# Performance work log

Hardware: AMD Instinct MI355X
Metric: run time of the kernel (lower is better)

The kernel has to match this reference:

```python
import jax, jax.numpy as jnp
import numpy as np
from jax import lax

IMAGE_SIZE = 1280
STRIDE = 32
FMP = IMAGE_SIZE // STRIDE          # 40
BPC = 5                             # boxes per cell (5 anchors)
NUM_CLASSES = 80
NMS_THRESH = 0.5
CONF_THRESH = 0.3
N_BOX = FMP * FMP * BPC             # 8000 candidates
ANCHOR_SIZE = np.array([[17, 25], [55, 75], [92, 206], [202, 21], [289, 311]], dtype=np.float32)


def _make_anchors():
    # generate_anchors: per-cell (x,y) grid repeated for each of BPC anchors, tiled anchor wh
    ys, xs = jnp.meshgrid(jnp.arange(FMP, dtype=jnp.float32), jnp.arange(FMP, dtype=jnp.float32), indexing='ij')
    xy = jnp.stack([xs, ys], axis=-1).reshape(-1, 1, 2)                       # [HW,1,2]
    anchor_xy = jnp.broadcast_to(xy, (FMP * FMP, BPC, 2)).reshape(-1, 2)      # [N,2]
    anchor_wh = jnp.broadcast_to(jnp.asarray(ANCHOR_SIZE)[None], (FMP * FMP, BPC, 2)).reshape(-1, 2)
    return jnp.concatenate([anchor_xy, anchor_wh], axis=-1)                   # [N,4]


def setup_inputs() -> dict:
    key = jax.random.key(0)
    k = jax.random.split(key, 5)
    return {
        'cls_feat': jax.random.normal(k[0], (1, 512, FMP, FMP), jnp.float32),
        'reg_feat': jax.random.normal(k[1], (1, 512, FMP, FMP), jnp.float32),
        'w_obj': jax.random.normal(k[2], (BPC, 512), jnp.float32) * 0.02,
        'b_obj': jnp.zeros((BPC,), jnp.float32),
        'w_cls': jax.random.normal(k[3], (NUM_CLASSES * BPC, 512), jnp.float32) * 0.02,
        'b_cls': jnp.zeros((NUM_CLASSES * BPC,), jnp.float32),
        'w_reg': jax.random.normal(k[4], (4 * BPC, 512), jnp.float32) * 0.02,
        'b_reg': jnp.zeros((4 * BPC,), jnp.float32),
    }


def reference(cls_feat, reg_feat, w_obj, b_obj, w_cls, b_cls, w_reg, b_reg):
    # 1x1 convs as channel contractions, already permuted to NHWC like permute(0,2,3,1)
    obj = (jnp.einsum('bchw,oc->bhwo', reg_feat, w_obj) + b_obj).reshape(-1, 1)            # [N,1]
    cls = (jnp.einsum('bchw,oc->bhwo', cls_feat, w_cls) + b_cls).reshape(-1, NUM_CLASSES)  # [N,C]
    reg = (jnp.einsum('bchw,oc->bhwo', reg_feat, w_reg) + b_reg).reshape(-1, 4)            # [N,4]

    scores = jnp.sqrt(jax.nn.sigmoid(obj) * jax.nn.sigmoid(cls))                           # [N,C]

    # decode_boxes
    anchors = _make_anchors()
    ctr = (jax.nn.sigmoid(reg[:, :2]) + anchors[:, :2]) * STRIDE
    wh = jnp.exp(reg[:, 2:]) * anchors[:, 2:]
    bboxes = jnp.concatenate([ctr - wh * 0.5, ctr + wh * 0.5], axis=-1)                    # [N,4] x1y1x2y2

    # postprocess: per-box best class + confidence filter
    labels = jnp.argmax(scores, axis=1)
    score = jnp.take_along_axis(scores, labels[:, None], axis=1)[:, 0]
    valid = score >= CONF_THRESH

    # faithful to original nms(): it re-interprets decoded x1y1x2y2 as cxcywh before IoU
    b2 = jnp.concatenate([bboxes[:, :2] - bboxes[:, 2:] * 0.5,
                          bboxes[:, :2] + bboxes[:, 2:] * 0.5], axis=-1)

    # greedy per-class NMS == global greedy with cross-class IoU gated to 0
    order = jnp.argsort(-score)
    bs = b2[order]
    ls = labels[order]
    vs = valid[order]
    areas = (bs[:, 2] - bs[:, 0]) * (bs[:, 3] - bs[:, 1])
    xx1 = jnp.maximum(bs[:, None, 0], bs[None, :, 0])
    yy1 = jnp.maximum(bs[:, None, 1], bs[None, :, 1])
    xx2 = jnp.minimum(bs[:, None, 2], bs[None, :, 2])
    yy2 = jnp.minimum(bs[:, None, 3], bs[None, :, 3])
    inter = jnp.maximum(1e-10, xx2 - xx1) * jnp.maximum(1e-10, yy2 - yy1)
    iou = inter / (areas[:, None] + areas[None, :] - inter + 1e-14)                        # [N,N]
    same = ls[:, None] == ls[None, :]

    idx = jnp.arange(N_BOX)

    def body(k, supp):
        active = vs[k] & jnp.logical_not(supp[k])
        row = active & (iou[k] > NMS_THRESH) & same[k] & (idx > k)
        return supp | row

    supp = lax.fori_loop(0, N_BOX, body, jnp.zeros(N_BOX, bool))
    keep = jnp.zeros(N_BOX, bool).at[order].set(vs & jnp.logical_not(supp))

    # fixed-size masked outputs (original returns variable-length filtered arrays)
    return bboxes, score, labels, keep
```

## Files before the change

### kernel.cpp

```cpp
#include <hip/hip_runtime.h>
#include <math.h>

#define FMPX 40
#define NPOS 1600
#define NCLS 80
#define NBOX 8000
#define KDIM 512
#define CAP  256

__constant__ float c_aw[5] = {17.f, 55.f, 92.f, 202.f, 289.f};
__constant__ float c_ah[5] = {25.f, 75.f, 206.f, 21.f, 311.f};

__device__ __forceinline__ float sigf(float x) { return 1.0f / (1.0f + expf(-x)); }

__global__ __launch_bounds__(256) void k_gemm(
    const float* __restrict__ cls_feat, const float* __restrict__ reg_feat,
    const float* __restrict__ w_obj, const float* __restrict__ b_obj,
    const float* __restrict__ w_cls, const float* __restrict__ b_cls,
    const float* __restrict__ w_reg, const float* __restrict__ b_reg,
    float* __restrict__ clsRaw,
    float* __restrict__ roRaw)
{
    __shared__ float Ws[16 * KDIM];
    const int mTile = blockIdx.x;
    const int nTile = blockIdx.y;
    const int hw0   = mTile * 64;
    const bool isCls = (nTile < 25);
    const float* feat = isCls ? cls_feat : reg_feat;

    const int pos = threadIdx.x & 63;
    const int og  = threadIdx.x >> 6;

    const float* ap = feat + hw0 + pos;

    float A0[8], A1[8];
#pragma unroll
    for (int t = 0; t < 8; t++) A0[t] = ap[t * NPOS];
#pragma unroll
    for (int t = 0; t < 8; t++) A1[t] = ap[(8 + t) * NPOS];

    for (int i = threadIdx.x * 4; i < 16 * KDIM; i += 256 * 4) {
        int r = i >> 9, k = i & 511;
        const float* src;
        bool valid = true;
        if (isCls) {
            src = w_cls + (nTile * 16 + r) * KDIM + k;
        } else {
            int o = (nTile - 25) * 16 + r;
            if (o < 5)       src = w_obj + o * KDIM + k;
            else if (o < 25) src = w_reg + (o - 5) * KDIM + k;
            else           { src = w_obj; valid = false; }
        }
        float4 v = valid ? *(const float4*)src : make_float4(0.f, 0.f, 0.f, 0.f);
        *(float4*)&Ws[i] = v;
    }

    float bias[4];
    bool ok[4];
#pragma unroll
    for (int j = 0; j < 4; j++) {
        int r = og * 4 + j;
        if (isCls) {
            bias[j] = b_cls[nTile * 16 + r]; ok[j] = true;
        } else {
            int o = (nTile - 25) * 16 + r;
            if (o < 5)       { bias[j] = b_obj[o];     ok[j] = true; }
            else if (o < 25) { bias[j] = b_reg[o - 5]; ok[j] = true; }
            else             { bias[j] = 0.0f;         ok[j] = false; }
        }
    }

    __syncthreads();

    float acc[4] = {0.f, 0.f, 0.f, 0.f};
    const float* wsBase = &Ws[(og * 4) * KDIM];

    for (int kk = 0; kk < KDIM - 16; kk += 16) {
#pragma unroll
        for (int j = 0; j < 4; j++) {
            const float* wp = wsBase + j * KDIM + kk;
            acc[j] += A0[0] * wp[0]; acc[j] += A0[1] * wp[1];
            acc[j] += A0[2] * wp[2]; acc[j] += A0[3] * wp[3];
            acc[j] += A0[4] * wp[4]; acc[j] += A0[5] * wp[5];
            acc[j] += A0[6] * wp[6]; acc[j] += A0[7] * wp[7];
        }
#pragma unroll
        for (int t = 0; t < 8; t++) A0[t] = ap[(kk + 16 + t) * NPOS];
#pragma unroll
        for (int j = 0; j < 4; j++) {
            const float* wp = wsBase + j * KDIM + kk + 8;
            acc[j] += A1[0] * wp[0]; acc[j] += A1[1] * wp[1];
            acc[j] += A1[2] * wp[2]; acc[j] += A1[3] * wp[3];
            acc[j] += A1[4] * wp[4]; acc[j] += A1[5] * wp[5];
            acc[j] += A1[6] * wp[6]; acc[j] += A1[7] * wp[7];
        }
#pragma unroll
        for (int t = 0; t < 8; t++) A1[t] = ap[(kk + 24 + t) * NPOS];
    }
    {
        const int kk = KDIM - 16;
#pragma unroll
        for (int j = 0; j < 4; j++) {
            const float* wp = wsBase + j * KDIM + kk;
            acc[j] += A0[0] * wp[0]; acc[j] += A0[1] * wp[1];
            acc[j] += A0[2] * wp[2]; acc[j] += A0[3] * wp[3];
            acc[j] += A0[4] * wp[4]; acc[j] += A0[5] * wp[5];
            acc[j] += A0[6] * wp[6]; acc[j] += A0[7] * wp[7];
        }
#pragma unroll
        for (int j = 0; j < 4; j++) {
            const float* wp = wsBase + j * KDIM + kk + 8;
            acc[j] += A1[0] * wp[0]; acc[j] += A1[1] * wp[1];
            acc[j] += A1[2] * wp[2]; acc[j] += A1[3] * wp[3];
            acc[j] += A1[4] * wp[4]; acc[j] += A1[5] * wp[5];
            acc[j] += A1[6] * wp[6]; acc[j] += A1[7] * wp[7];
        }
    }

    const int hw = hw0 + pos;
    if (isCls) {
        float4 rv = make_float4(acc[0] + bias[0], acc[1] + bias[1],
                                acc[2] + bias[2], acc[3] + bias[3]);
        *(float4*)&clsRaw[hw * 400 + nTile * 16 + og * 4] = rv;
    } else {
#pragma unroll
        for (int j = 0; j < 4; j++) {
            int o = (nTile - 25) * 16 + og * 4 + j;
            if (ok[j]) roRaw[hw * 25 + o] = acc[j] + bias[j];
        }
    }
}

__global__ __launch_bounds__(256) void k_box(
    const float* __restrict__ clsRaw, const float* __restrict__ roRaw,
    float* __restrict__ out,
    float4* __restrict__ nmsBox, float* __restrict__ nmsArea,
    float2* __restrict__ sl)
{
    const int n = blockIdx.x * 4 + (threadIdx.x >> 6);
    const int lane = threadIdx.x & 63;
    const int hw = n / 5, a = n % 5;

    const float sobj = sigf(roRaw[hw * 25 + a]);
    const float* cbase = clsRaw + hw * 400 + a * 80;

    const int l4 = (lane < 20) ? lane : 19;
    float4 cs = *(const float4*)(cbase + l4 * 4);

    float s0 = sqrtf(sobj * sigf(cs.x));
    float s1 = sqrtf(sobj * sigf(cs.y));
    float s2 = sqrtf(sobj * sigf(cs.z));
    float s3 = sqrtf(sobj * sigf(cs.w));
    float v = s0; int bi = l4 * 4;
    if (s1 > v) { v = s1; bi = l4 * 4 + 1; }
    if (s2 > v) { v = s2; bi = l4 * 4 + 2; }
    if (s3 > v) { v = s3; bi = l4 * 4 + 3; }
    if (lane >= 20) { v = -1.0f; bi = 0x7FFFFFFF; }

#pragma unroll
    for (int off = 32; off >= 1; off >>= 1) {
        float ov = __shfl_xor(v, off);
        int   oi = __shfl_xor(bi, off);
        if (ov > v || (ov == v && oi < bi)) { v = ov; bi = oi; }
    }

    if (lane == 0) {
        const float* rp = roRaw + hw * 25 + 5 + a * 4;
        float r0 = rp[0], r1 = rp[1], r2 = rp[2], r3 = rp[3];
        float gx = (float)(hw % FMPX), gy = (float)(hw / FMPX);
        float cx = (sigf(r0) + gx) * 32.0f;
        float cy = (sigf(r1) + gy) * 32.0f;
        float wv = expf(r2) * c_aw[a];
        float hv = expf(r3) * c_ah[a];
        float x1 = cx - wv * 0.5f, y1 = cy - hv * 0.5f;
        float x2 = cx + wv * 0.5f, y2 = cy + hv * 0.5f;

        out[n * 4 + 0] = x1; out[n * 4 + 1] = y1;
        out[n * 4 + 2] = x2; out[n * 4 + 3] = y2;
        out[32000 + n] = v;
        out[40000 + n] = (float)bi;
        out[48000 + n] = 0.0f;
        sl[n] = make_float2(v, (float)bi);

        float nx1 = x1 - x2 * 0.5f, ny1 = y1 - y2 * 0.5f;
        float nx2 = x1 + x2 * 0.5f, ny2 = y1 + y2 * 0.5f;
        nmsBox[n]  = make_float4(nx1, ny1, nx2, ny2);
        nmsArea[n] = (nx2 - nx1) * (ny2 - ny1);
    }
}

__global__ __launch_bounds__(256) void k_nms(
    const float2* __restrict__ sl,
    const float4* __restrict__ nmsBox, const float* __restrict__ nmsArea,
    float* __restrict__ keepOut)
{
    const int c = blockIdx.x;

    __shared__ float ss[CAP];
    __shared__ int   si[CAP];
    __shared__ float rx1[CAP], ry1[CAP], rx2[CAP], ry2[CAP], rar[CAP];
    __shared__ int   rid[CAP];
    __shared__ int   cnt;

    if (threadIdx.x == 0) cnt = 0;
    __syncthreads();

#pragma unroll 4
    for (int i = threadIdx.x; i < NBOX; i += 256) {
        float2 p = sl[i];
        if (p.x >= 0.3f && (int)p.y == c) {
            int q = atomicAdd(&cnt, 1);
            if (q < CAP) { ss[q] = p.x; si[q] = i; }
        }
    }
    __syncthreads();

    int m = cnt;
    if (m > CAP) m = CAP;

    {
        const int t = threadIdx.x;
        if (t < m) {
            const float msc = ss[t];
            const int   mid = si[t];
            const float4 b = nmsBox[mid];
            const float  a = nmsArea[mid];
            int rank = 0;
            for (int j = 0; j < m; j++) {
                float sj = ss[j]; int ij = si[j];
                if (sj > msc || (sj == msc && ij < mid)) rank++;
            }
            rx1[rank] = b.x; ry1[rank] = b.y;
            rx2[rank] = b.z; ry2[rank] = b.w;
            rar[rank] = a;   rid[rank] = mid;
        }
    }
    __syncthreads();

    if (threadIdx.x >= 64) return;
    const int lane = threadIdx.x;

    bool act[4];
    float x1[4], y1[4], x2[4], y2[4], ar[4];
#pragma unroll
    for (int r = 0; r < 4; r++) {
        const int p = r * 64 + lane;
        act[r] = (p < m);
        if (act[r]) {
            x1[r] = rx1[p]; y1[r] = ry1[p];
            x2[r] = rx2[p]; y2[r] = ry2[p]; ar[r] = rar[p];
        } else {
            x1[r] = 0.f; y1[r] = 0.f; x2[r] = 0.f; y2[r] = 0.f; ar[r] = 0.f;
        }
    }

    unsigned long long M0 = __ballot(act[0]);
    unsigned long long M1 = __ballot(act[1]);
    unsigned long long M2 = __ballot(act[2]);
    unsigned long long M3 = __ballot(act[3]);

    for (int k = 0; k < m; k++) {
        const int w = k >> 6;
        const unsigned long long Mw = (w == 0) ? M0 : (w == 1) ? M1
                                    : (w == 2) ? M2 : M3;
        if (!((Mw >> (k & 63)) & 1ULL)) continue;

        const float kx1 = rx1[k], ky1 = ry1[k];
        const float kx2 = rx2[k], ky2 = ry2[k], ka = rar[k];
        if (lane == 0) keepOut[rid[k]] = 1.0f;

#pragma unroll
        for (int r = 0; r < 4; r++) {
            if (act[r]) {
                float xx1 = fmaxf(kx1, x1[r]);
                float yy1 = fmaxf(ky1, y1[r]);
                float xx2 = fminf(kx2, x2[r]);
                float yy2 = fminf(ky2, y2[r]);
                float inter = fmaxf(1e-10f, xx2 - xx1) * fmaxf(1e-10f, yy2 - yy1);
                float iou = inter / ((ka + ar[r] - inter) + 1e-14f);
                if (iou > 0.5f) act[r] = false;
            }
        }
        M0 = __ballot(act[0]); M1 = __ballot(act[1]);
        M2 = __ballot(act[2]); M3 = __ballot(act[3]);
    }
}

extern "C" void kernel_launch(void* const* d_in, const int* in_sizes, int n_in,
                              void* d_out, int out_size, void* d_ws, size_t ws_size,
                              hipStream_t stream) {
    const float* cls_feat = (const float*)d_in[0];
    const float* reg_feat = (const float*)d_in[1];
    const float* w_obj    = (const float*)d_in[2];
    const float* b_obj    = (const float*)d_in[3];
    const float* w_cls    = (const float*)d_in[4];
    const float* b_cls    = (const float*)d_in[5];
    const float* w_reg    = (const float*)d_in[6];
    const float* b_reg    = (const float*)d_in[7];

    float* out = (float*)d_out;
    float* ws  = (float*)d_ws;

    float*  clsRaw    = ws;
    float*  roRaw     = ws + 640000;
    float4* nmsBox    = (float4*)(ws + 680000);
    float*  nmsArea   = ws + 712000;
    float2* sl        = (float2*)(ws + 720000);

    k_gemm<<<dim3(25, 27), 256, 0, stream>>>(cls_feat, reg_feat,
                                             w_obj, b_obj, w_cls, b_cls, w_reg, b_reg,
                                             clsRaw, roRaw);
    k_box<<<NBOX / 4, 256, 0, stream>>>(clsRaw, roRaw, out, nmsBox, nmsArea, sl);
    k_nms<<<NCLS, 256, 0, stream>>>(sl, nmsBox, nmsArea, out + 48000);
}
```

Measured before the change: 162.7 us.

## Precompute per-class IoU suppression bitmask matrix for NMS in parallel

The per-class NMS kernel now has all 256 threads build an IoU>0.5 bitmask matrix (one 64-bit word per 64 candidates per row) in shared memory before the greedy pass. The serial greedy loop then picks the next survivor with ctz on scalar masks and clears suppressed bits with AND-NOT, so it no longer does IoU math and ballots for every candidate. This replaces serial per-step arithmetic with a parallel O(m^2) precompute, at the cost of extra shared memory and computing IoU pairs that greedy NMS would have skipped.

```diff
diff --git a/kernel.cpp b/kernel.cpp
--- a/kernel.cpp
+++ b/kernel.cpp
@@ -196,11 +196,13 @@
 {
     const int c = blockIdx.x;
 
-    __shared__ float ss[CAP];
-    __shared__ int   si[CAP];
-    __shared__ float rx1[CAP], ry1[CAP], rx2[CAP], ry2[CAP], rar[CAP];
-    __shared__ int   rid[CAP];
-    __shared__ int   cnt;
+    __shared__ float  ss[CAP];
+    __shared__ int    si[CAP];
+    __shared__ float4 sb4[CAP];
+    __shared__ float  sar[CAP];
+    __shared__ int    rid[CAP];
+    __shared__ unsigned long long erow[4][CAP];
+    __shared__ int    cnt;
 
     if (threadIdx.x == 0) cnt = 0;
     __syncthreads();
@@ -230,9 +232,34 @@
                 float sj = ss[j]; int ij = si[j];
                 if (sj > msc || (sj == msc && ij < mid)) rank++;
             }
-            rx1[rank] = b.x; ry1[rank] = b.y;
-            rx2[rank] = b.z; ry2[rank] = b.w;
-            rar[rank] = a;   rid[rank] = mid;
+            sb4[rank] = b; sar[rank] = a; rid[rank] = mid;
+        }
+    }
+    __syncthreads();
+
+    {
+        const int p = threadIdx.x;
+        if (p < m) {
+            const float4 pb = sb4[p];
+            const float  pa = sar[p];
+#pragma unroll
+            for (int w = 0; w < 4; w++) {
+                unsigned long long ew = 0ull;
+                const int j0 = w * 64;
+                const int j1 = (m < j0 + 64) ? m : (j0 + 64);
+                for (int j = j0; j < j1; j++) {
+                    float4 bj = sb4[j];
+                    float  aj = sar[j];
+                    float xx1 = fmaxf(pb.x, bj.x);
+                    float yy1 = fmaxf(pb.y, bj.y);
+                    float xx2 = fminf(pb.z, bj.z);
+                    float yy2 = fminf(pb.w, bj.w);
+                    float inter = fmaxf(1e-10f, xx2 - xx1) * fmaxf(1e-10f, yy2 - yy1);
+                    float iou = inter / ((pa + aj - inter) + 1e-14f);
+                    if (iou > 0.5f) ew |= (1ull << (j & 63));
+                }
+                erow[w][p] = ew;
+            }
         }
     }
     __syncthreads();
@@ -240,49 +267,32 @@
     if (threadIdx.x >= 64) return;
     const int lane = threadIdx.x;
 
-    bool act[4];
-    float x1[4], y1[4], x2[4], y2[4], ar[4];
-#pragma unroll
-    for (int r = 0; r < 4; r++) {
-        const int p = r * 64 + lane;
-        act[r] = (p < m);
-        if (act[r]) {
-            x1[r] = rx1[p]; y1[r] = ry1[p];
-            x2[r] = rx2[p]; y2[r] = ry2[p]; ar[r] = rar[p];
-        } else {
-            x1[r] = 0.f; y1[r] = 0.f; x2[r] = 0.f; y2[r] = 0.f; ar[r] = 0.f;
-        }
-    }
-
-    unsigned long long M0 = __ballot(act[0]);
-    unsigned long long M1 = __ballot(act[1]);
-    unsigned long long M2 = __ballot(act[2]);
-    unsigned long long M3 = __ballot(act[3]);
-
-    for (int k = 0; k < m; k++) {
-        const int w = k >> 6;
-        const unsigned long long Mw = (w == 0) ? M0 : (w == 1) ? M1
-                                    : (w == 2) ? M2 : M3;
-        if (!((Mw >> (k & 63)) & 1ULL)) continue;
-
-        const float kx1 = rx1[k], ky1 = ry1[k];
-        const float kx2 = rx2[k], ky2 = ry2[k], ka = rar[k];
-        if (lane == 0) keepOut[rid[k]] = 1.0f;
-
-#pragma unroll
-        for (int r = 0; r < 4; r++) {
-            if (act[r]) {
-                float xx1 = fmaxf(kx1, x1[r]);
-                float yy1 = fmaxf(ky1, y1[r]);
-                float xx2 = fminf(kx2, x2[r]);
-                float yy2 = fminf(ky2, y2[r]);
-                float inter = fmaxf(1e-10f, xx2 - xx1) * fmaxf(1e-10f, yy2 - yy1);
-                float iou = inter / ((ka + ar[r] - inter) + 1e-14f);
-                if (iou > 0.5f) act[r] = false;
-            }
-        }
-        M0 = __ballot(act[0]); M1 = __ballot(act[1]);
-        M2 = __ballot(act[2]); M3 = __ballot(act[3]);
+    unsigned long long A[4];
+#pragma unroll
+    for (int w = 0; w < 4; w++) {
+        int lo = w * 64;
+        A[w] = (m >= lo + 64) ? ~0ull
+             : (m > lo ? ((1ull << (m - lo)) - 1ull) : 0ull);
+    }
+
+    for (int guard = 0; guard < m; guard++) {
+        int k = -1;
+#pragma unroll
+        for (int w = 0; w < 4; w++)
+            if (k < 0 && A[w] != 0ull) k = w * 64 + (int)__builtin_ctzll(A[w]);
+        if (k < 0) break;
+
+        unsigned long long r0 = erow[0][k];
+        unsigned long long r1 = erow[1][k];
+        unsigned long long r2 = erow[2][k];
+        unsigned long long r3 = erow[3][k];
+        int kid = rid[k];
+        if (lane == 0) keepOut[kid] = 1.0f;
+
+#pragma unroll
+        for (int w = 0; w < 4; w++)
+            if ((k >> 6) == w) A[w] &= ~(1ull << (k & 63));
+        A[0] &= ~r0; A[1] &= ~r1; A[2] &= ~r2; A[3] &= ~r3;
     }
 }
 
```

Measured after the change: 158.1 us. 2.9% less time.
